# Kernel tuning notes

Measured on AMD Instinct MI355X. Metric: run time of the kernel, lower is better.

## Reference

```python
import jax, jax.numpy as jnp
import numpy as np

B, NQ, NK, D, H = 4, 2048, 2048, 1024, 16
DH = D // H
SCALE = DH ** -0.5


def setup_inputs() -> dict:
    key = jax.random.key(0)
    ks = jax.random.split(key, 8)
    s = 0.02
    return {
        "x_q": jax.random.normal(ks[0], (B, NQ, D), dtype=jnp.float32),
        "x_kv": jax.random.normal(ks[1], (B, NK, D), dtype=jnp.float32),
        "Wq": jax.random.normal(ks[2], (D, D), dtype=jnp.float32) * s,
        "bq": jnp.zeros((D,), dtype=jnp.float32),
        "Wkv": jax.random.normal(ks[3], (D, 2 * D), dtype=jnp.float32) * s,
        "bkv": jnp.zeros((2 * D,), dtype=jnp.float32),
        "Wp": jax.random.normal(ks[4], (D, D), dtype=jnp.float32) * s,
        "bp": jnp.zeros((D,), dtype=jnp.float32),
    }


def reference(x_q, x_kv, Wq, bq, Wkv, bkv, Wp, bp):
    # q: [B, H, Nq, Dh]
    q = (x_q @ Wq + bq).reshape(B, NQ, H, DH).transpose(0, 2, 1, 3)
    kv = (x_kv @ Wkv + bkv).reshape(B, NK, 2, H, DH)
    k = kv[:, :, 0].transpose(0, 2, 1, 3)  # [B, H, Nk, Dh]
    v = kv[:, :, 1].transpose(0, 2, 1, 3)  # [B, H, Nk, Dh]
    attn = jnp.einsum("bhqd,bhkd->bhqk", q, k) * SCALE  # [B, H, Nq, Nk]
    attn = jax.nn.softmax(attn, axis=-1)
    out = jnp.einsum("bhqk,bhkd->bhqd", attn, v)  # [B, H, Nq, Dh]
    out = out.transpose(0, 2, 1, 3).reshape(B, NQ, D)
    return jnp.nan_to_num(x_q + out @ Wp + bp)
```

## Files before the change

### kernel.cpp

```cpp
#include <hip/hip_runtime.h>
#include <hip/hip_bf16.h>

#define B_   4
#define NQ_  2048
#define NK_  2048
#define D_   1024
#define H_   16
#define DH_  64
#define SCALE_ 0.125f

typedef __attribute__((ext_vector_type(8))) __bf16 bf16x8;
typedef __attribute__((ext_vector_type(4))) float  f32x4;

typedef const __attribute__((address_space(1))) unsigned int* gas1p;
typedef __attribute__((address_space(3))) unsigned int*       las3p;

__device__ __forceinline__ f32x4 mfma16(bf16x8 a, bf16x8 b, f32x4 c) {
  return __builtin_amdgcn_mfma_f32_16x16x32_bf16(a, b, c, 0, 0, 0);
}
__device__ __forceinline__ void gload_lds16(const void* g, void* l) {
  __builtin_amdgcn_global_load_lds((gas1p)g, (las3p)l, 16, 0, 0);
}
__device__ __forceinline__ float nn_(float x) {
  if (__builtin_isnan(x)) return 0.0f;
  if (__builtin_isinf(x)) return x > 0.f ? 3.402823466e38f : -3.402823466e38f;
  return x;
}
__device__ __forceinline__ float exp2_(float x) {
#if __has_builtin(__builtin_amdgcn_exp2f)
  return __builtin_amdgcn_exp2f(x);
#else
  return __expf(x * 0.69314718056f);
#endif
}

__global__ __launch_bounds__(256) void cvt_bf16_k(const float* __restrict__ s,
                                                  __bf16* __restrict__ d, int n) {
  int i = (blockIdx.x * blockDim.x + threadIdx.x) << 2;
  if (i >= n) return;
  float4 v = *(const float4*)(s + i);
  __bf16 o[4] __attribute__((aligned(8))) = {(__bf16)v.x, (__bf16)v.y, (__bf16)v.z, (__bf16)v.w};
  *(uint2*)(d + i) = *(uint2*)o;
}

__global__ __launch_bounds__(256) void transpose_cvt_k(const float* __restrict__ src,
                                                       __bf16* __restrict__ dst,
                                                       int K, int N) {
  __shared__ float t[32][33];
  int n0 = blockIdx.x * 32, k0 = blockIdx.y * 32;
  int x = threadIdx.x, y0 = threadIdx.y;
  for (int yy = y0; yy < 32; yy += 8)
    t[yy][x] = src[(size_t)(k0 + yy) * N + n0 + x];
  __syncthreads();
  for (int yy = y0; yy < 32; yy += 8)
    dst[(size_t)(n0 + yy) * K + k0 + x] = (__bf16)t[x][yy];
}

template <bool OUT_BF16, bool RES>
__global__ __launch_bounds__(256) void gemm_bt_k(const __bf16* __restrict__ A,
                                                 const __bf16* __restrict__ Bt,
                                                 const float* __restrict__ bias,
                                                 const float* __restrict__ res,
                                                 void* __restrict__ out,
                                                 int M, int N, int K) {
  __shared__ __attribute__((aligned(16))) __bf16 As[128 * 32];
  __shared__ __attribute__((aligned(16))) __bf16 Bs[128 * 32];
  const int tid = threadIdx.x, lane = tid & 63, wid = tid >> 6;
  const int wr = wid >> 1, wc = wid & 1;
  const int g = lane >> 4, lr = lane & 15;
  const int m0 = blockIdx.y * 128, n0 = blockIdx.x * 128;

  const f32x4 zero4 = {0.f, 0.f, 0.f, 0.f};
  f32x4 acc[4][4];
#pragma unroll
  for (int m = 0; m < 4; m++)
#pragma unroll
    for (int n = 0; n < 4; n++) acc[m][n] = zero4;

  for (int k0 = 0; k0 < K; k0 += 32) {
    __syncthreads();
#pragma unroll
    for (int i = 0; i < 2; i++) {
      int c = wid * 128 + i * 64 + lane;
      gload_lds16(A + (size_t)(m0 + (c >> 2)) * K + k0 + ((c & 3) << 3),
                  (char*)As + wid * 2048 + i * 1024);
      gload_lds16(Bt + (size_t)(n0 + (c >> 2)) * K + k0 + ((c & 3) << 3),
                  (char*)Bs + wid * 2048 + i * 1024);
    }
    __syncthreads();

    bf16x8 af[4], bfv[4];
#pragma unroll
    for (int m = 0; m < 4; m++)
      af[m] = *(const bf16x8*)(As + (wr * 64 + m * 16 + lr) * 32 + g * 8);
#pragma unroll
    for (int n = 0; n < 4; n++)
      bfv[n] = *(const bf16x8*)(Bs + (wc * 64 + n * 16 + lr) * 32 + g * 8);
#pragma unroll
    for (int m = 0; m < 4; m++)
#pragma unroll
      for (int n = 0; n < 4; n++) acc[m][n] = mfma16(af[m], bfv[n], acc[m][n]);
  }

#pragma unroll
  for (int m = 0; m < 4; m++) {
    int row = m0 + wr * 64 + m * 16 + g * 4;
#pragma unroll
    for (int n = 0; n < 4; n++) {
      int col = n0 + wc * 64 + n * 16 + lr;
      float bv = bias[col];
#pragma unroll
      for (int r = 0; r < 4; r++) {
        size_t idx = (size_t)(row + r) * N + col;
        float v = acc[m][n][r] + bv;
        if (RES) v = nn_(v + res[idx]);
        if (OUT_BF16) ((__bf16*)out)[idx] = (__bf16)v;
        else          ((float*)out)[idx] = v;
      }
    }
  }
}

__global__ __launch_bounds__(256) void reorder_v_k(const __bf16* __restrict__ kv,
                                                   __bf16* __restrict__ vt) {
  __shared__ __attribute__((aligned(16))) __bf16 t[64][72];
  int bh = blockIdx.y, b = bh >> 4, h = bh & 15;
  int kk0 = blockIdx.x * 64;
  int tid = threadIdx.x;
#pragma unroll
  for (int i = 0; i < 2; i++) {
    int c = tid + i * 256;
    int kk = c >> 3, dc = c & 7;
    const __bf16* src = kv + (size_t)(b * NK_ + kk0 + kk) * 2048 + 1024 + h * 64 + dc * 8;
    *(float4*)&t[kk][dc * 8] = *(const float4*)src;
  }
  __syncthreads();
#pragma unroll
  for (int i = 0; i < 2; i++) {
    int c = tid + i * 256;
    int d = c >> 3, gch = c & 7;
    int s = gch ^ (d & 7);
    __bf16 tmp[8] __attribute__((aligned(16)));
#pragma unroll
    for (int j = 0; j < 8; j++) tmp[j] = t[s * 8 + j][d];
    __bf16* dst = vt + ((size_t)bh * 64 + d) * (size_t)NK_ + kk0 + gch * 8;
    *(float4*)dst = *(float4*)tmp;
  }
}

__global__ __launch_bounds__(256) void attn_k(const __bf16* __restrict__ Qg,
                                              const __bf16* __restrict__ KVg,
                                              const __bf16* __restrict__ Vt,
                                              __bf16* __restrict__ AO) {
  __shared__ __attribute__((aligned(16))) __bf16 Kt[2][64 * 64];
  __shared__ __attribute__((aligned(16))) __bf16 Vl[2][64 * 64];
  __shared__ __attribute__((aligned(16))) __bf16 Pl[4][16 * 64];
  const int tid = threadIdx.x, lane = tid & 63, wid = tid >> 6;
  const int g = lane >> 4, lr = lane & 15;
  const int bid = blockIdx.x;
  const int bh = bid & 63, b = bh >> 4, h = bh & 15;
  const int qbase = (bid >> 6) * 64 + wid * 16;
  const float C2 = SCALE_ * 1.44269504089f;

  bf16x8 qf[2];
  {
    const __bf16* qp = Qg + ((size_t)(b * NQ_ + qbase + lr)) * 1024 + h * 64 + g * 8;
    qf[0] = *(const bf16x8*)qp;
    qf[1] = *(const bf16x8*)(qp + 32);
  }

  const f32x4 zero4 = {0.f, 0.f, 0.f, 0.f};
  f32x4 po[4];
#pragma unroll
  for (int df = 0; df < 4; df++) po[df] = zero4;
  float m2 = -1e30f, l = 0.f;

  char* pw = (char*)&Pl[wid][0];
  const int swz = (lr & 7) << 4;
  int wa[4], ra[2];
#pragma unroll
  for (int n = 0; n < 4; n++) wa[n] = lr * 128 + ((n * 32 + g * 8) ^ swz);
#pragma unroll
  for (int ks = 0; ks < 2; ks++) ra[ks] = lr * 128 + ((ks * 64 + g * 16) ^ swz);

  const int kkw = wid * 16 + (lane >> 3);
  const int cc = lane & 7;
  const __bf16* Ksrc = KVg + (size_t)b * NK_ * 2048 + h * 64;
  const __bf16* Vsrc = Vt + (size_t)bh * 64 * (size_t)NK_;

#define STAGE_(bi, kv0)                                                              \
  {                                                                                  \
    _Pragma("unroll") for (int i = 0; i < 2; i++) {                                  \
      int kk = kkw + i * 8;                                                          \
      gload_lds16(Ksrc + (size_t)((kv0) + kk) * 2048 + ((cc ^ (kk & 7)) << 3),       \
                  (char*)&Kt[bi][0] + wid * 2048 + i * 1024);                        \
      gload_lds16(Vsrc + (size_t)kk * NK_ + (kv0) + (cc << 3),                       \
                  (char*)&Vl[bi][0] + wid * 2048 + i * 1024);                        \
    }                                                                                \
  }

  int cur = 0;
  STAGE_(0, 0);

  for (int t = 0; t < NK_ / 64; ++t) {
    const int kv0 = t << 6;
    if (t < NK_ / 64 - 1) {
      STAGE_(cur ^ 1, kv0 + 64);
      asm volatile("s_waitcnt vmcnt(4)" ::: "memory");
    } else {
      asm volatile("s_waitcnt vmcnt(0)" ::: "memory");
    }
    asm volatile("s_barrier" ::: "memory");

    const char* Kb = (const char*)&Kt[cur][0];
    const char* Vb = (const char*)&Vl[cur][0];

    f32x4 sa[4];
    __builtin_amdgcn_s_setprio(1);
#pragma unroll
    for (int n = 0; n < 4; n++) {
      sa[n] = zero4;
      int kk = n * 16 + lr;
#pragma unroll
      for (int ds = 0; ds < 2; ds++) {
        bf16x8 kf = *(const bf16x8*)(Kb + kk * 128 + ((ds * 64 + g * 16) ^ ((kk & 7) << 4)));
        sa[n] = mfma16(kf, qf[ds], sa[n]);
      }
    }
    __builtin_amdgcn_s_setprio(0);

    float mx = -1e30f;
#pragma unroll
    for (int n = 0; n < 4; n++)
#pragma unroll
      for (int r = 0; r < 4; r++) mx = fmaxf(mx, sa[n][r]);
    mx = fmaxf(mx, __shfl_xor(mx, 16));
    mx = fmaxf(mx, __shfl_xor(mx, 32));
    mx *= C2;

    if (__any(mx > m2 + 11.0f)) {
      float mn = fmaxf(m2, mx);
      float alpha = exp2_(m2 - mn);
      m2 = mn;
      l *= alpha;
#pragma unroll
      for (int r = 0; r < 4; r++) {
        float ar = __shfl(alpha, g * 4 + r);
#pragma unroll
        for (int df = 0; df < 4; df++) po[df][r] *= ar;
      }
    }

    float rs = 0.f;
#pragma unroll
    for (int n = 0; n < 4; n++) {
      union { __bf16 hh[4]; uint2 u; } qd;
#pragma unroll
      for (int r = 0; r < 4; r++) {
        float p = exp2_(fmaf(sa[n][r], C2, -m2));
        rs += p;
        qd.hh[r] = (__bf16)p;
      }
      *(uint2*)(pw + wa[n]) = qd.u;
    }
    rs += __shfl_xor(rs, 16);
    rs += __shfl_xor(rs, 32);
    l += rs;

    bf16x8 pa[2];
#pragma unroll
    for (int ks = 0; ks < 2; ks++) pa[ks] = *(const bf16x8*)(pw + ra[ks]);

    __builtin_amdgcn_s_setprio(1);
#pragma unroll
    for (int df = 0; df < 4; df++) {
      int d = df * 16 + lr;
#pragma unroll
      for (int ks = 0; ks < 2; ks++) {
        bf16x8 vf = *(const bf16x8*)(Vb + d * 128 + ((ks * 64 + g * 16) ^ ((d & 7) << 4)));
        po[df] = mfma16(pa[ks], vf, po[df]);
      }
    }
    __builtin_amdgcn_s_setprio(0);

    asm volatile("s_barrier" ::: "memory");
    cur ^= 1;
  }

  float inv = 1.0f / l;
#pragma unroll
  for (int r = 0; r < 4; r++) {
    float ir = __shfl(inv, g * 4 + r);
    size_t row = (size_t)(b * NQ_ + qbase + g * 4 + r);
#pragma unroll
    for (int df = 0; df < 4; df++)
      AO[row * 1024 + h * 64 + df * 16 + lr] = (__bf16)(po[df][r] * ir);
  }
#undef STAGE_
}

extern "C" void kernel_launch(void* const* d_in, const int* in_sizes, int n_in,
                              void* d_out, int out_size, void* d_ws, size_t ws_size,
                              hipStream_t stream) {
  (void)in_sizes; (void)n_in; (void)out_size; (void)ws_size;
  const float* x_q  = (const float*)d_in[0];
  const float* x_kv = (const float*)d_in[1];
  const float* Wq   = (const float*)d_in[2];
  const float* bq   = (const float*)d_in[3];
  const float* Wkv  = (const float*)d_in[4];
  const float* bkv  = (const float*)d_in[5];
  const float* Wp   = (const float*)d_in[6];
  const float* bp   = (const float*)d_in[7];

  char* w = (char*)d_ws;
  __bf16* xq_bf  = (__bf16*)w; w += (size_t)8388608 * 2;
  __bf16* xkv_bf = (__bf16*)w; w += (size_t)8388608 * 2;
  __bf16* Wq_t   = (__bf16*)w; w += (size_t)1048576 * 2;
  __bf16* Wkv_t  = (__bf16*)w; w += (size_t)2097152 * 2;
  __bf16* Wp_t   = (__bf16*)w; w += (size_t)1048576 * 2;
  __bf16* Q_bf   = (__bf16*)w; w += (size_t)8388608 * 2;
  __bf16* KV_bf  = (__bf16*)w; w += (size_t)16777216 * 2;
  __bf16* Vt     = (__bf16*)w; w += (size_t)8388608 * 2;
  __bf16* AO     = (__bf16*)w; w += (size_t)8388608 * 2;

  cvt_bf16_k<<<8192, 256, 0, stream>>>(x_q, xq_bf, 8388608);
  cvt_bf16_k<<<8192, 256, 0, stream>>>(x_kv, xkv_bf, 8388608);
  transpose_cvt_k<<<dim3(32, 32), dim3(32, 8), 0, stream>>>(Wq, Wq_t, 1024, 1024);
  transpose_cvt_k<<<dim3(64, 32), dim3(32, 8), 0, stream>>>(Wkv, Wkv_t, 1024, 2048);
  transpose_cvt_k<<<dim3(32, 32), dim3(32, 8), 0, stream>>>(Wp, Wp_t, 1024, 1024);

  gemm_bt_k<true, false><<<dim3(8, 64), 256, 0, stream>>>(xq_bf, Wq_t, bq, nullptr, Q_bf, 8192, 1024, 1024);
  gemm_bt_k<true, false><<<dim3(16, 64), 256, 0, stream>>>(xkv_bf, Wkv_t, bkv, nullptr, KV_bf, 8192, 2048, 1024);
  reorder_v_k<<<dim3(32, 64), 256, 0, stream>>>(KV_bf, Vt);
  attn_k<<<2048, 256, 0, stream>>>(Q_bf, KV_bf, Vt, AO);
  gemm_bt_k<false, true><<<dim3(8, 64), 256, 0, stream>>>(AO, Wp_t, bp, x_q, d_out, 8192, 1024, 1024);
}
```

Baseline: 405.2 us.

## Replace GEMM with double-buffered 256-row tiles and fold softmax scale into Wq

```diff
diff --git a/kernel.cpp b/kernel.cpp
--- a/kernel.cpp
+++ b/kernel.cpp
@@ -45,7 +45,7 @@
 
 __global__ __launch_bounds__(256) void transpose_cvt_k(const float* __restrict__ src,
                                                        __bf16* __restrict__ dst,
-                                                       int K, int N) {
+                                                       int K, int N, float scale) {
   __shared__ float t[32][33];
   int n0 = blockIdx.x * 32, k0 = blockIdx.y * 32;
   int x = threadIdx.x, y0 = threadIdx.y;
@@ -53,66 +53,112 @@
     t[yy][x] = src[(size_t)(k0 + yy) * N + n0 + x];
   __syncthreads();
   for (int yy = y0; yy < 32; yy += 8)
-    dst[(size_t)(n0 + yy) * K + k0 + x] = (__bf16)t[x][yy];
-}
-
-template <bool OUT_BF16, bool RES>
-__global__ __launch_bounds__(256) void gemm_bt_k(const __bf16* __restrict__ A,
-                                                 const __bf16* __restrict__ Bt,
-                                                 const float* __restrict__ bias,
-                                                 const float* __restrict__ res,
-                                                 void* __restrict__ out,
-                                                 int M, int N, int K) {
-  __shared__ __attribute__((aligned(16))) __bf16 As[128 * 32];
-  __shared__ __attribute__((aligned(16))) __bf16 Bs[128 * 32];
+    dst[(size_t)(n0 + yy) * K + k0 + x] = (__bf16)(t[x][yy] * scale);
+}
+
+template <int BN, bool OUT_BF16, bool RES>
+__global__ __launch_bounds__(512, 2) void gemm256_k(const __bf16* __restrict__ A,
+                                                    const __bf16* __restrict__ Bt,
+                                                    const float* __restrict__ bias, float bscale,
+                                                    const float* __restrict__ res,
+                                                    void* __restrict__ out,
+                                                    int M, int N, int K) {
+  constexpr int BM = 256, BK = 64;
+  constexpr int ALOADS = 4;
+  constexpr int BLOADS = (BN == 256) ? 4 : 2;
+  constexpr int NRq = BN / 128;
+  __shared__ __attribute__((aligned(16))) __bf16 Al[2][BM * BK];
+  __shared__ __attribute__((aligned(16))) __bf16 Bl[2][BN * BK];
+
   const int tid = threadIdx.x, lane = tid & 63, wid = tid >> 6;
-  const int wr = wid >> 1, wc = wid & 1;
+  const int wr = wid >> 2, wc = wid & 3;
   const int g = lane >> 4, lr = lane & 15;
-  const int m0 = blockIdx.y * 128, n0 = blockIdx.x * 128;
+  const int m0 = blockIdx.y * BM, n0 = blockIdx.x * BN;
+
+  auto stageA = [&](int dbuf, int k0, int j) {
+    int c = j * 512 + tid;
+    gload_lds16(A + (size_t)(m0 + (c >> 3)) * K + k0 + ((c & 7) << 3),
+                (char*)&Al[dbuf][0] + ((j * 512 + (wid << 6)) << 4));
+  };
+  auto stageB = [&](int dbuf, int k0, int j) {
+    int c = j * 512 + tid;
+    gload_lds16(Bt + (size_t)(n0 + (c >> 3)) * K + k0 + ((c & 7) << 3),
+                (char*)&Bl[dbuf][0] + ((j * 512 + (wid << 6)) << 4));
+  };
 
   const f32x4 zero4 = {0.f, 0.f, 0.f, 0.f};
-  f32x4 acc[4][4];
-#pragma unroll
-  for (int m = 0; m < 4; m++)
-#pragma unroll
-    for (int n = 0; n < 4; n++) acc[m][n] = zero4;
-
-  for (int k0 = 0; k0 < K; k0 += 32) {
-    __syncthreads();
-#pragma unroll
-    for (int i = 0; i < 2; i++) {
-      int c = wid * 128 + i * 64 + lane;
-      gload_lds16(A + (size_t)(m0 + (c >> 2)) * K + k0 + ((c & 3) << 3),
-                  (char*)As + wid * 2048 + i * 1024);
-      gload_lds16(Bt + (size_t)(n0 + (c >> 2)) * K + k0 + ((c & 3) << 3),
-                  (char*)Bs + wid * 2048 + i * 1024);
-    }
-    __syncthreads();
-
-    bf16x8 af[4], bfv[4];
-#pragma unroll
-    for (int m = 0; m < 4; m++)
-      af[m] = *(const bf16x8*)(As + (wr * 64 + m * 16 + lr) * 32 + g * 8);
-#pragma unroll
-    for (int n = 0; n < 4; n++)
-      bfv[n] = *(const bf16x8*)(Bs + (wc * 64 + n * 16 + lr) * 32 + g * 8);
-#pragma unroll
-    for (int m = 0; m < 4; m++)
-#pragma unroll
-      for (int n = 0; n < 4; n++) acc[m][n] = mfma16(af[m], bfv[n], acc[m][n]);
-  }
-
-#pragma unroll
-  for (int m = 0; m < 4; m++) {
-    int row = m0 + wr * 64 + m * 16 + g * 4;
-#pragma unroll
-    for (int n = 0; n < 4; n++) {
-      int col = n0 + wc * 64 + n * 16 + lr;
-      float bv = bias[col];
-#pragma unroll
-      for (int r = 0; r < 4; r++) {
+  f32x4 acc[8][BN / 64];
+#pragma unroll
+  for (int m = 0; m < 8; m++)
+#pragma unroll
+    for (int n = 0; n < BN / 64; n++) acc[m][n] = zero4;
+
+#pragma unroll
+  for (int j = 0; j < ALOADS; ++j) stageA(0, 0, j);
+#pragma unroll
+  for (int j = 0; j < BLOADS; ++j) stageB(0, 0, j);
+  asm volatile("s_waitcnt vmcnt(0)" ::: "memory");
+  asm volatile("s_barrier" ::: "memory");
+
+  const int KT = K >> 6;
+  for (int t = 0; t < KT; ++t) {
+    const int buf = t & 1, nbuf = buf ^ 1;
+    const int k1 = (t + 1) << 6;
+    const bool pf = (t + 1 < KT);
+    const __bf16* Ab = &Al[buf][0];
+    const __bf16* Bb = &Bl[buf][0];
+    bf16x8 af[2][4], bv[2][NRq];
+#pragma unroll
+    for (int q = 0; q < 4; ++q) {
+      const int rh = q >> 1, ch = q & 1;
+      if ((q & 1) == 0) {
+#pragma unroll
+        for (int ks = 0; ks < 2; ++ks)
+#pragma unroll
+          for (int m = 0; m < 4; ++m)
+            af[ks][m] = *(const bf16x8*)(Ab + (wr * 128 + rh * 64 + m * 16 + lr) * 64 + ks * 32 + g * 8);
+      }
+#pragma unroll
+      for (int ks = 0; ks < 2; ++ks)
+#pragma unroll
+        for (int n = 0; n < NRq; ++n)
+          bv[ks][n] = *(const bf16x8*)(Bb + (wc * (BN / 4) + ch * (BN / 8) + n * 16 + lr) * 64 + ks * 32 + g * 8);
+      if (pf) {
+        if (q == 0) { stageA(nbuf, k1, 0); stageA(nbuf, k1, 1); if (BLOADS == 4) stageB(nbuf, k1, 0); }
+        if (q == 1) { stageA(nbuf, k1, 2); stageA(nbuf, k1, 3); if (BLOADS == 4) stageB(nbuf, k1, 1); }
+        if (q == 2) {
+          if (BLOADS == 4) { stageB(nbuf, k1, 2); stageB(nbuf, k1, 3); }
+          else             { stageB(nbuf, k1, 0); stageB(nbuf, k1, 1); }
+        }
+      }
+      asm volatile("s_barrier" ::: "memory");
+      asm volatile("s_waitcnt lgkmcnt(0)" ::: "memory");
+      __builtin_amdgcn_sched_barrier(0);
+      __builtin_amdgcn_s_setprio(1);
+#pragma unroll
+      for (int m = 0; m < 4; ++m)
+#pragma unroll
+        for (int n = 0; n < NRq; ++n)
+#pragma unroll
+          for (int ks = 0; ks < 2; ++ks)
+            acc[rh * 4 + m][ch * NRq + n] = mfma16(af[ks][m], bv[ks][n], acc[rh * 4 + m][ch * NRq + n]);
+      __builtin_amdgcn_s_setprio(0);
+      if (q == 3 && pf) asm volatile("s_waitcnt vmcnt(0)" ::: "memory");
+      asm volatile("s_barrier" ::: "memory");
+    }
+  }
+
+#pragma unroll
+  for (int Mi = 0; Mi < 8; ++Mi) {
+    int row = m0 + wr * 128 + Mi * 16 + g * 4;
+#pragma unroll
+    for (int Ni = 0; Ni < BN / 64; ++Ni) {
+      int col = n0 + wc * (BN / 4) + Ni * 16 + lr;
+      float bvv = bias[col] * bscale;
+#pragma unroll
+      for (int r = 0; r < 4; ++r) {
         size_t idx = (size_t)(row + r) * N + col;
-        float v = acc[m][n][r] + bv;
+        float v = acc[Mi][Ni][r] + bvv;
         if (RES) v = nn_(v + res[idx]);
         if (OUT_BF16) ((__bf16*)out)[idx] = (__bf16)v;
         else          ((float*)out)[idx] = v;
@@ -160,7 +206,6 @@
   const int bid = blockIdx.x;
   const int bh = bid & 63, b = bh >> 4, h = bh & 15;
   const int qbase = (bid >> 6) * 64 + wid * 16;
-  const float C2 = SCALE_ * 1.44269504089f;
 
   bf16x8 qf[2];
   {
@@ -236,7 +281,6 @@
       for (int r = 0; r < 4; r++) mx = fmaxf(mx, sa[n][r]);
     mx = fmaxf(mx, __shfl_xor(mx, 16));
     mx = fmaxf(mx, __shfl_xor(mx, 32));
-    mx *= C2;
 
     if (__any(mx > m2 + 11.0f)) {
       float mn = fmaxf(m2, mx);
@@ -257,7 +301,7 @@
       union { __bf16 hh[4]; uint2 u; } qd;
 #pragma unroll
       for (int r = 0; r < 4; r++) {
-        float p = exp2_(fmaf(sa[n][r], C2, -m2));
+        float p = exp2_(sa[n][r] - m2);
         rs += p;
         qd.hh[r] = (__bf16)p;
       }
@@ -266,6 +310,8 @@
     rs += __shfl_xor(rs, 16);
     rs += __shfl_xor(rs, 32);
     l += rs;
+
+    asm volatile("s_waitcnt lgkmcnt(0)" ::: "memory");
 
     bf16x8 pa[2];
 #pragma unroll
@@ -323,15 +369,17 @@
   __bf16* Vt     = (__bf16*)w; w += (size_t)8388608 * 2;
   __bf16* AO     = (__bf16*)w; w += (size_t)8388608 * 2;
 
+  const float C2 = SCALE_ * 1.44269504089f;
+
   cvt_bf16_k<<<8192, 256, 0, stream>>>(x_q, xq_bf, 8388608);
   cvt_bf16_k<<<8192, 256, 0, stream>>>(x_kv, xkv_bf, 8388608);
-  transpose_cvt_k<<<dim3(32, 32), dim3(32, 8), 0, stream>>>(Wq, Wq_t, 1024, 1024);
-  transpose_cvt_k<<<dim3(64, 32), dim3(32, 8), 0, stream>>>(Wkv, Wkv_t, 1024, 2048);
-  transpose_cvt_k<<<dim3(32, 32), dim3(32, 8), 0, stream>>>(Wp, Wp_t, 1024, 1024);
-
-  gemm_bt_k<true, false><<<dim3(8, 64), 256, 0, stream>>>(xq_bf, Wq_t, bq, nullptr, Q_bf, 8192, 1024, 1024);
-  gemm_bt_k<true, false><<<dim3(16, 64), 256, 0, stream>>>(xkv_bf, Wkv_t, bkv, nullptr, KV_bf, 8192, 2048, 1024);
+  transpose_cvt_k<<<dim3(32, 32), dim3(32, 8), 0, stream>>>(Wq, Wq_t, 1024, 1024, C2);
+  transpose_cvt_k<<<dim3(64, 32), dim3(32, 8), 0, stream>>>(Wkv, Wkv_t, 1024, 2048, 1.0f);
+  transpose_cvt_k<<<dim3(32, 32), dim3(32, 8), 0, stream>>>(Wp, Wp_t, 1024, 1024, 1.0f);
+
+  gemm256_k<128, true, false><<<dim3(8, 32), 512, 0, stream>>>(xq_bf, Wq_t, bq, C2, nullptr, Q_bf, 8192, 1024, 1024);
+  gemm256_k<256, true, false><<<dim3(8, 32), 512, 0, stream>>>(xkv_bf, Wkv_t, bkv, 1.0f, nullptr, KV_bf, 8192, 2048, 1024);
   reorder_v_k<<<dim3(32, 64), 256, 0, stream>>>(KV_bf, Vt);
   attn_k<<<2048, 256, 0, stream>>>(Q_bf, KV_bf, Vt, AO);
-  gemm_bt_k<false, true><<<dim3(8, 64), 256, 0, stream>>>(AO, Wp_t, bp, x_q, d_out, 8192, 1024, 1024);
-}
+  gemm256_k<128, false, true><<<dim3(8, 32), 512, 0, stream>>>(AO, Wp_t, bp, 1.0f, x_q, d_out, 8192, 1024, 1024);
+}
```

New measurement: 414.6 us. 2.3% more time.

## Triple-buffer GEMM with 256x128 tiles and fold softmax scale into Wq

Applied to the files above, without the earlier changes.

```diff
diff --git a/kernel.cpp b/kernel.cpp
--- a/kernel.cpp
+++ b/kernel.cpp
@@ -45,7 +45,7 @@
 
 __global__ __launch_bounds__(256) void transpose_cvt_k(const float* __restrict__ src,
                                                        __bf16* __restrict__ dst,
-                                                       int K, int N) {
+                                                       int K, int N, float scale) {
   __shared__ float t[32][33];
   int n0 = blockIdx.x * 32, k0 = blockIdx.y * 32;
   int x = threadIdx.x, y0 = threadIdx.y;
@@ -53,22 +53,39 @@
     t[yy][x] = src[(size_t)(k0 + yy) * N + n0 + x];
   __syncthreads();
   for (int yy = y0; yy < 32; yy += 8)
-    dst[(size_t)(n0 + yy) * K + k0 + x] = (__bf16)t[x][yy];
+    dst[(size_t)(n0 + yy) * K + k0 + x] = (__bf16)(t[x][yy] * scale);
 }
 
 template <bool OUT_BF16, bool RES>
-__global__ __launch_bounds__(256) void gemm_bt_k(const __bf16* __restrict__ A,
-                                                 const __bf16* __restrict__ Bt,
-                                                 const float* __restrict__ bias,
-                                                 const float* __restrict__ res,
-                                                 void* __restrict__ out,
-                                                 int M, int N, int K) {
-  __shared__ __attribute__((aligned(16))) __bf16 As[128 * 32];
-  __shared__ __attribute__((aligned(16))) __bf16 Bs[128 * 32];
+__global__ __launch_bounds__(512, 4) void gemm3p_k(const __bf16* __restrict__ A,
+                                                   const __bf16* __restrict__ Bt,
+                                                   const float* __restrict__ bias, float bscale,
+                                                   const float* __restrict__ res,
+                                                   void* __restrict__ out,
+                                                   int M, int N, int K) {
+  constexpr int BM = 256, BN = 128, BK = 32;
+  __shared__ __attribute__((aligned(16))) __bf16 Al[3][BM * BK];
+  __shared__ __attribute__((aligned(16))) __bf16 Bl[3][BN * BK];
   const int tid = threadIdx.x, lane = tid & 63, wid = tid >> 6;
   const int wr = wid >> 1, wc = wid & 1;
   const int g = lane >> 4, lr = lane & 15;
-  const int m0 = blockIdx.y * 128, n0 = blockIdx.x * 128;
+  const int m0 = blockIdx.y * BM, n0 = blockIdx.x * BN;
+
+  const int ca1 = tid + 512;
+  const int rowA0 = tid >> 2, rowA1 = ca1 >> 2, rowB = tid >> 2;
+  const __bf16* aSrc0 = A + (size_t)(m0 + rowA0) * K + (((tid & 3) ^ (rowA0 & 3)) << 3);
+  const __bf16* aSrc1 = A + (size_t)(m0 + rowA1) * K + (((ca1 & 3) ^ (rowA1 & 3)) << 3);
+  const __bf16* bSrc  = Bt + (size_t)(n0 + rowB) * K + (((tid & 3) ^ (rowB & 3)) << 3);
+  char* aDst0 = (char*)&Al[0][0] + (tid << 4);
+  char* aDst1 = (char*)&Al[0][0] + (ca1 << 4);
+  char* bDst  = (char*)&Bl[0][0] + (tid << 4);
+
+  const int swz = (lr & 3) << 4;
+  int offA[4], offB[4];
+#pragma unroll
+  for (int m = 0; m < 4; m++) offA[m] = (wr * 64 + m * 16 + lr) * 64 + ((g * 16) ^ swz);
+#pragma unroll
+  for (int n = 0; n < 4; n++) offB[n] = (wc * 64 + n * 16 + lr) * 64 + ((g * 16) ^ swz);
 
   const f32x4 zero4 = {0.f, 0.f, 0.f, 0.f};
   f32x4 acc[4][4];
@@ -77,42 +94,54 @@
 #pragma unroll
     for (int n = 0; n < 4; n++) acc[m][n] = zero4;
 
-  for (int k0 = 0; k0 < K; k0 += 32) {
-    __syncthreads();
-#pragma unroll
-    for (int i = 0; i < 2; i++) {
-      int c = wid * 128 + i * 64 + lane;
-      gload_lds16(A + (size_t)(m0 + (c >> 2)) * K + k0 + ((c & 3) << 3),
-                  (char*)As + wid * 2048 + i * 1024);
-      gload_lds16(Bt + (size_t)(n0 + (c >> 2)) * K + k0 + ((c & 3) << 3),
-                  (char*)Bs + wid * 2048 + i * 1024);
-    }
-    __syncthreads();
-
-    bf16x8 af[4], bfv[4];
+  gload_lds16(aSrc0, aDst0); gload_lds16(aSrc1, aDst1); gload_lds16(bSrc, bDst);
+  gload_lds16(aSrc0 + BK, aDst0 + 16384); gload_lds16(aSrc1 + BK, aDst1 + 16384);
+  gload_lds16(bSrc + BK, bDst + 8192);
+  asm volatile("s_waitcnt vmcnt(3)" ::: "memory");
+  __builtin_amdgcn_s_barrier();
+
+  const int KT = K / BK;
+  int cb = 0, b2 = 2;
+  for (int t = 0; t < KT; ++t) {
+    const char* Ab = (const char*)&Al[0][0] + cb * 16384;
+    const char* Bb = (const char*)&Bl[0][0] + cb * 8192;
+    bf16x8 af[4], bv[4];
+#pragma unroll
+    for (int m = 0; m < 4; m++) af[m] = *(const bf16x8*)(Ab + offA[m]);
+#pragma unroll
+    for (int n = 0; n < 4; n++) bv[n] = *(const bf16x8*)(Bb + offB[n]);
+    if (t < KT - 2) {
+      const int k2 = (t + 2) * BK;
+      gload_lds16(aSrc0 + k2, aDst0 + b2 * 16384);
+      gload_lds16(aSrc1 + k2, aDst1 + b2 * 16384);
+      gload_lds16(bSrc + k2, bDst + b2 * 8192);
+    }
+    asm volatile("s_waitcnt lgkmcnt(0)" ::: "memory");
+    __builtin_amdgcn_sched_barrier(0);
+    __builtin_amdgcn_s_setprio(1);
 #pragma unroll
     for (int m = 0; m < 4; m++)
-      af[m] = *(const bf16x8*)(As + (wr * 64 + m * 16 + lr) * 32 + g * 8);
-#pragma unroll
-    for (int n = 0; n < 4; n++)
-      bfv[n] = *(const bf16x8*)(Bs + (wc * 64 + n * 16 + lr) * 32 + g * 8);
-#pragma unroll
-    for (int m = 0; m < 4; m++)
-#pragma unroll
-      for (int n = 0; n < 4; n++) acc[m][n] = mfma16(af[m], bfv[n], acc[m][n]);
-  }
-
-#pragma unroll
-  for (int m = 0; m < 4; m++) {
-    int row = m0 + wr * 64 + m * 16 + g * 4;
-#pragma unroll
-    for (int n = 0; n < 4; n++) {
-      int col = n0 + wc * 64 + n * 16 + lr;
-      float bv = bias[col];
-#pragma unroll
-      for (int r = 0; r < 4; r++) {
+#pragma unroll
+      for (int n = 0; n < 4; n++) acc[m][n] = mfma16(af[m], bv[n], acc[m][n]);
+    __builtin_amdgcn_s_setprio(0);
+    if (t < KT - 2)       asm volatile("s_waitcnt vmcnt(3)" ::: "memory");
+    else if (t == KT - 2) asm volatile("s_waitcnt vmcnt(0)" ::: "memory");
+    if (t < KT - 1) __builtin_amdgcn_s_barrier();
+    cb = (cb == 2) ? 0 : cb + 1;
+    b2 = (b2 == 2) ? 0 : b2 + 1;
+  }
+
+#pragma unroll
+  for (int Mi = 0; Mi < 4; ++Mi) {
+    int row = m0 + wr * 64 + Mi * 16 + g * 4;
+#pragma unroll
+    for (int Ni = 0; Ni < 4; ++Ni) {
+      int col = n0 + wc * 64 + Ni * 16 + lr;
+      float bvv = bias[col] * bscale;
+#pragma unroll
+      for (int r = 0; r < 4; ++r) {
         size_t idx = (size_t)(row + r) * N + col;
-        float v = acc[m][n][r] + bv;
+        float v = acc[Mi][Ni][r] + bvv;
         if (RES) v = nn_(v + res[idx]);
         if (OUT_BF16) ((__bf16*)out)[idx] = (__bf16)v;
         else          ((float*)out)[idx] = v;
@@ -160,7 +189,6 @@
   const int bid = blockIdx.x;
   const int bh = bid & 63, b = bh >> 4, h = bh & 15;
   const int qbase = (bid >> 6) * 64 + wid * 16;
-  const float C2 = SCALE_ * 1.44269504089f;
 
   bf16x8 qf[2];
   {
@@ -236,7 +264,6 @@
       for (int r = 0; r < 4; r++) mx = fmaxf(mx, sa[n][r]);
     mx = fmaxf(mx, __shfl_xor(mx, 16));
     mx = fmaxf(mx, __shfl_xor(mx, 32));
-    mx *= C2;
 
     if (__any(mx > m2 + 11.0f)) {
       float mn = fmaxf(m2, mx);
@@ -257,7 +284,7 @@
       union { __bf16 hh[4]; uint2 u; } qd;
 #pragma unroll
       for (int r = 0; r < 4; r++) {
-        float p = exp2_(fmaf(sa[n][r], C2, -m2));
+        float p = exp2_(sa[n][r] - m2);
         rs += p;
         qd.hh[r] = (__bf16)p;
       }
@@ -266,6 +293,8 @@
     rs += __shfl_xor(rs, 16);
     rs += __shfl_xor(rs, 32);
     l += rs;
+
+    asm volatile("s_waitcnt lgkmcnt(0)" ::: "memory");
 
     bf16x8 pa[2];
 #pragma unroll
@@ -323,15 +352,17 @@
   __bf16* Vt     = (__bf16*)w; w += (size_t)8388608 * 2;
   __bf16* AO     = (__bf16*)w; w += (size_t)8388608 * 2;
 
+  const float C2 = SCALE_ * 1.44269504089f;
+
   cvt_bf16_k<<<8192, 256, 0, stream>>>(x_q, xq_bf, 8388608);
   cvt_bf16_k<<<8192, 256, 0, stream>>>(x_kv, xkv_bf, 8388608);
-  transpose_cvt_k<<<dim3(32, 32), dim3(32, 8), 0, stream>>>(Wq, Wq_t, 1024, 1024);
-  transpose_cvt_k<<<dim3(64, 32), dim3(32, 8), 0, stream>>>(Wkv, Wkv_t, 1024, 2048);
-  transpose_cvt_k<<<dim3(32, 32), dim3(32, 8), 0, stream>>>(Wp, Wp_t, 1024, 1024);
-
-  gemm_bt_k<true, false><<<dim3(8, 64), 256, 0, stream>>>(xq_bf, Wq_t, bq, nullptr, Q_bf, 8192, 1024, 1024);
-  gemm_bt_k<true, false><<<dim3(16, 64), 256, 0, stream>>>(xkv_bf, Wkv_t, bkv, nullptr, KV_bf, 8192, 2048, 1024);
+  transpose_cvt_k<<<dim3(32, 32), dim3(32, 8), 0, stream>>>(Wq, Wq_t, 1024, 1024, C2);
+  transpose_cvt_k<<<dim3(64, 32), dim3(32, 8), 0, stream>>>(Wkv, Wkv_t, 1024, 2048, 1.0f);
+  transpose_cvt_k<<<dim3(32, 32), dim3(32, 8), 0, stream>>>(Wp, Wp_t, 1024, 1024, 1.0f);
+
+  gemm3p_k<true, false><<<dim3(8, 32), 512, 0, stream>>>(xq_bf, Wq_t, bq, C2, nullptr, Q_bf, 8192, 1024, 1024);
+  gemm3p_k<true, false><<<dim3(16, 32), 512, 0, stream>>>(xkv_bf, Wkv_t, bkv, 1.0f, nullptr, KV_bf, 8192, 2048, 1024);
   reorder_v_k<<<dim3(32, 64), 256, 0, stream>>>(KV_bf, Vt);
   attn_k<<<2048, 256, 0, stream>>>(Q_bf, KV_bf, Vt, AO);
-  gemm_bt_k<false, true><<<dim3(8, 64), 256, 0, stream>>>(AO, Wp_t, bp, x_q, d_out, 8192, 1024, 1024);
-}
+  gemm3p_k<false, true><<<dim3(8, 32), 512, 0, stream>>>(AO, Wp_t, bp, 1.0f, x_q, d_out, 8192, 1024, 1024);
+}
```

New measurement: 390.5 us. 3.6% less time.
